# Optimization experiments

Hardware: AMD Instinct MI355X
Metric: run time of the kernel (lower is better)

## Reference

```python
import jax, jax.numpy as jnp
import numpy as np

DISC = 10  # discretizer bins
EPS = 1e-5


def _discretize(x):
    # stand-in for sklearn discretizer: uniform bins over [-3, 3] for N(0,1) data
    t = jnp.clip(jnp.floor((x + 3.0) / 6.0 * DISC), 0, DISC - 1)
    return jax.lax.stop_gradient(t).astype(jnp.int32)


def _levenshtein(tokens, features):
    # tokens: [B, L] int32, features: [Nf, F] int32 -> [B, Nf] float32
    B, L = tokens.shape
    Nf, F = features.shape
    idx = jnp.arange(L + 1, dtype=jnp.int32)
    prev0 = jnp.broadcast_to(idx, (B, Nf, L + 1)).astype(jnp.int32)

    def step(carry, fc):
        prev, j = carry  # prev: [B, Nf, L+1]
        cost = (tokens[:, None, :] != fc[None, :, None]).astype(jnp.int32)  # [B,Nf,L]
        a_rest = jnp.minimum(prev[..., 1:] + 1, prev[..., :-1] + cost)
        a0 = jnp.full((B, Nf, 1), j + 1, dtype=jnp.int32)
        a = jnp.concatenate([a0, a_rest], axis=-1)
        # cur[i] = min(a[i], cur[i-1]+1) == i + cummin(a - i)
        cur = jax.lax.cummin(a - idx, axis=2) + idx
        return (cur, j + 1), None

    (prev, _), _ = jax.lax.scan(step, (prev0, jnp.int32(0)), features.T)
    return prev[..., L].astype(jnp.float32)


def _correlations(tokens, features, L):
    # interpolate each length-F feature to length L (linear, cast to int), then pearson corr
    Nf, F = features.shape
    x_old = jnp.linspace(0.0, 1.0, F)
    x_new = jnp.linspace(0.0, 1.0, L)
    fi = jax.vmap(lambda f: jnp.interp(x_new, x_old, f.astype(jnp.float32)))(features)
    fi = fi.astype(jnp.int32).astype(jnp.float32)  # [Nf, L] (astype(int) in original)
    rf = tokens.astype(jnp.float32)  # [B, L]
    fc = fi - fi.mean(axis=-1, keepdims=True)
    rc = rf - rf.mean(axis=-1, keepdims=True)
    num = jnp.einsum('nl,bl->bn', fc, rc)
    den = jnp.linalg.norm(fc, axis=-1)[None, :] * jnp.linalg.norm(rc, axis=-1)[:, None]
    return jnp.where(den > 0, num / jnp.where(den > 0, den, 1.0), 0.0)  # [B, Nf]


def setup_inputs() -> dict:
    key = jax.random.key(0)
    k1, k2, k3 = jax.random.split(key, 3)
    B, L, Nf, F, D = 64, 512, 1024, 16, 512
    x = jax.random.normal(k1, (B, L, 1), dtype=jnp.float32)
    features = jax.random.randint(k2, (Nf, F), 0, DISC, dtype=jnp.int32)
    fan_in = 2 * 3  # in_channels * kernel
    std = np.sqrt(2.0 / (1.0 + 0.01 ** 2) / fan_in)  # kaiming, leaky_relu
    conv_w = jax.random.normal(k3, (D, 2, 3), dtype=jnp.float32) * std
    return {"x": x, "features": features, "conv_w": conv_w}


def reference(x, features, conv_w):
    B, L, _ = x.shape
    tokens = _discretize(x[..., 0])  # [B, L] int32
    dist = _levenshtein(tokens, features)  # [B, Nf]
    corr = _correlations(tokens, features, L)  # [B, Nf]
    # normalize distances over feature axis (dim=1), unbiased=False
    m = dist.mean(axis=1, keepdims=True)
    v = dist.var(axis=1, keepdims=True)
    dbg = (dist - m) / jnp.sqrt(v + EPS)
    feats2 = jnp.stack([corr, dbg], axis=1)  # [B, 2, Nf] (corr first, as torch.cat)
    # circular conv1d, kernel 3, padding 1, no bias
    inp = jnp.pad(feats2, ((0, 0), (0, 0), (1, 1)), mode='wrap')
    out = jax.lax.conv_general_dilated(inp, conv_w, (1,), 'VALID',
                                       dimension_numbers=('NCH', 'OIH', 'NCH'))  # [B, D, Nf]
    # dropout in eval mode = identity
    return jnp.transpose(out, (0, 2, 1))  # [B, Nf, D]
```

## Files before the change

kernel.cpp:

```cpp
#include <hip/hip_runtime.h>
#include <math.h>

#define NB 64
#define LL 512
#define NF 1024
#define FF 16
#define DD 512

__global__ __launch_bounds__(256) void k_prep(
    const float* __restrict__ x, const int* __restrict__ feat,
    unsigned* __restrict__ tok_pk, int* __restrict__ tsum, int* __restrict__ tsumsq,
    unsigned char* __restrict__ fiTp, int* __restrict__ fsum, int* __restrict__ fsumsq) {
  int tid = threadIdx.x;
  int blk = blockIdx.x;
  if (blk < 64) {
    int b = blk;
    __shared__ unsigned char tc[LL];
    __shared__ int redS[4], redQ[4];
    int s = 0, q = 0;
    #pragma unroll
    for (int k = 0; k < 2; ++k) {
      int l = tid + k * 256;
      float xf = x[b * LL + l];
      float c = (xf + 3.0f) / 6.0f * 10.0f;
      float tf = fminf(fmaxf(floorf(c), 0.0f), 9.0f);
      int t = (int)tf;
      tc[l] = (unsigned char)t;
      s += t; q += t * t;
    }
    #pragma unroll
    for (int o = 32; o > 0; o >>= 1) { s += __shfl_xor(s, o); q += __shfl_xor(q, o); }
    if ((tid & 63) == 0) { redS[tid >> 6] = s; redQ[tid >> 6] = q; }
    __syncthreads();
    if (tid < 128) {
      unsigned u = (unsigned)tc[tid * 4] | ((unsigned)tc[tid * 4 + 1] << 8) |
                   ((unsigned)tc[tid * 4 + 2] << 16) | ((unsigned)tc[tid * 4 + 3] << 24);
      tok_pk[b * 128 + tid] = u;
    }
    if (tid == 0) {
      tsum[b] = redS[0] + redS[1] + redS[2] + redS[3];
      tsumsq[b] = redQ[0] + redQ[1] + redQ[2] + redQ[3];
    }
  } else if (blk < 576) {
    int l = blk - 64;
    double u = (double)l * 15.0 / 511.0;
    int j = (int)u; if (j > 14) j = 14;
    double w = u - (double)j;
    size_t base = (size_t)(l >> 2) * 4096 + (size_t)(l & 3);
    #pragma unroll
    for (int k = 0; k < 4; ++k) {
      int n = tid + k * 256;
      int f0 = feat[n * FF + j], f1 = feat[n * FF + j + 1];
      int v = (int)((double)f0 + w * (double)(f1 - f0));
      fiTp[base + (size_t)n * 4] = (unsigned char)v;
    }
  } else {
    int n = blk - 576;
    __shared__ int fr[FF];
    __shared__ int rs[4], rq[4];
    if (tid < FF) fr[tid] = feat[n * FF + tid];
    __syncthreads();
    int s = 0, q = 0;
    #pragma unroll
    for (int k = 0; k < 2; ++k) {
      int l = tid + k * 256;
      double u = (double)l * 15.0 / 511.0;
      int j = (int)u; if (j > 14) j = 14;
      double w = u - (double)j;
      int f0 = fr[j], f1 = fr[j + 1];
      int v = (int)((double)f0 + w * (double)(f1 - f0));
      s += v; q += v * v;
    }
    #pragma unroll
    for (int o = 32; o > 0; o >>= 1) { s += __shfl_xor(s, o); q += __shfl_xor(q, o); }
    if ((tid & 63) == 0) { rs[tid >> 6] = s; rq[tid >> 6] = q; }
    __syncthreads();
    if (tid == 0) {
      fsum[n] = rs[0] + rs[1] + rs[2] + rs[3];
      fsumsq[n] = rq[0] + rq[1] + rq[2] + rq[3];
    }
  }
}

__global__ __launch_bounds__(256) void k_levc(
    const unsigned* __restrict__ tok_pk, const int* __restrict__ feat,
    const unsigned* __restrict__ fiTp4,
    const int* __restrict__ fsum, const int* __restrict__ fsumsq,
    const int* __restrict__ tsum, const int* __restrict__ tsumsq,
    float* __restrict__ dist, float* __restrict__ corr) {
  int tid = threadIdx.x;
  int b = blockIdx.x >> 2;
  int n = ((blockIdx.x & 3) << 8) + tid;
  __shared__ unsigned lt[128];
  __shared__ unsigned peq[10 * 256];
  if (tid < 128) lt[tid] = tok_pk[b * 128 + tid];
  int f[FF];
  const int4* f4 = reinterpret_cast<const int4*>(feat + (size_t)n * FF);
  #pragma unroll
  for (int j = 0; j < 4; ++j) {
    int4 v = f4[j];
    f[j * 4 + 0] = v.x; f[j * 4 + 1] = v.y; f[j * 4 + 2] = v.z; f[j * 4 + 3] = v.w;
  }
  #pragma unroll
  for (int c = 0; c < 10; ++c) {
    unsigned m = 0;
    #pragma unroll
    for (int j = 0; j < 16; ++j) m |= (f[j] == c) ? (1u << j) : 0u;
    peq[c * 256 + tid] = m;
  }
  __syncthreads();
  unsigned VP = 0xFFFFu, VN = 0u;
  int score = 16;
  int acc = 0;
  for (int l4 = 0; l4 < 128; ++l4) {
    unsigned u = lt[l4];
    unsigned g = fiTp4[l4 * 1024 + n];
    #pragma unroll
    for (int k = 0; k < 4; ++k) {
      unsigned t = (u >> (8 * k)) & 0xffu;
      unsigned Eq = peq[t * 256 + tid];
      unsigned D0 = (((Eq & VP) + VP) ^ VP) | Eq | VN;
      unsigned HP = VN | ~(D0 | VP);
      unsigned HN = D0 & VP;
      score += (int)((HP >> 15) & 1u);
      score -= (int)((HN >> 15) & 1u);
      unsigned X = (HP << 1) | 1u;
      VP = (HN << 1) | ~(D0 | X);
      VN = D0 & X;
      unsigned fi = (g >> (8 * k)) & 0xffu;
      acc += (int)(t * fi);
    }
  }
  dist[b * NF + n] = (float)score;
  float ts = (float)tsum[b];
  float rv = fmaxf((float)tsumsq[b] - ts * ts * (1.0f / 512.0f), 0.0f);
  float rn = sqrtf(rv);
  float fs = (float)fsum[n];
  float fv = fmaxf((float)fsumsq[n] - fs * fs * (1.0f / 512.0f), 0.0f);
  float den = sqrtf(fv) * rn;
  float num = (float)acc - fs * ts * (1.0f / 512.0f);
  corr[b * NF + n] = (den > 0.0f) ? (num / den) : 0.0f;
}

__global__ __launch_bounds__(256) void k_dstats(
    const float* __restrict__ dist, float* __restrict__ dstats) {
  int b = blockIdx.x, tid = threadIdx.x;
  double s = 0.0, q = 0.0;
  #pragma unroll
  for (int k = 0; k < 4; ++k) {
    float v = dist[b * NF + tid + k * 256];
    s += (double)v; q += (double)v * (double)v;
  }
  #pragma unroll
  for (int o = 32; o > 0; o >>= 1) { s += __shfl_xor(s, o); q += __shfl_xor(q, o); }
  __shared__ double rs[4], rq[4];
  if ((tid & 63) == 0) { rs[tid >> 6] = s; rq[tid >> 6] = q; }
  __syncthreads();
  if (tid == 0) {
    double S = rs[0] + rs[1] + rs[2] + rs[3];
    double Q = rq[0] + rq[1] + rq[2] + rq[3];
    double m = S * (1.0 / 1024.0);
    double var = Q * (1.0 / 1024.0) - m * m;
    dstats[b * 2] = (float)m;
    dstats[b * 2 + 1] = (float)(1.0 / sqrt(var + 1e-5));
  }
}

__global__ __launch_bounds__(256) void k_conv(
    const float* __restrict__ corr, const float* __restrict__ dist,
    const float* __restrict__ dstats, const float* __restrict__ w,
    float* __restrict__ out) {
  int chunk = blockIdx.x;
  int b = blockIdx.y;
  int tid = threadIdx.x;
  __shared__ float cs[66], ds_[66];
  float m = dstats[b * 2], inv = dstats[b * 2 + 1];
  if (tid < 66) {
    int ng = (chunk * 64 + tid - 1 + NF) & (NF - 1);
    cs[tid] = corr[b * NF + ng];
    ds_[tid] = (dist[b * NF + ng] - m) * inv;
  }
  __syncthreads();
  int d0 = tid * 2;
  float w0[6], w1[6];
  #pragma unroll
  for (int i = 0; i < 6; ++i) {
    w0[i] = w[d0 * 6 + i];
    w1[i] = w[(d0 + 1) * 6 + i];
  }
  const int nb = chunk * 64;
  for (int n = 0; n < 64; ++n) {
    float v0 = cs[n], v1 = cs[n + 1], v2 = cs[n + 2];
    float v3 = ds_[n], v4 = ds_[n + 1], v5 = ds_[n + 2];
    float o0 = w0[0]*v0 + w0[1]*v1 + w0[2]*v2 + w0[3]*v3 + w0[4]*v4 + w0[5]*v5;
    float o1 = w1[0]*v0 + w1[1]*v1 + w1[2]*v2 + w1[3]*v3 + w1[4]*v4 + w1[5]*v5;
    float2* op = (float2*)(out + ((size_t)(b * NF + nb + n)) * DD + d0);
    *op = make_float2(o0, o1);
  }
}

extern "C" void kernel_launch(void* const* d_in, const int* in_sizes, int n_in,
                              void* d_out, int out_size, void* d_ws, size_t ws_size,
                              hipStream_t stream) {
  const float* x = (const float*)d_in[0];
  const int* feat = (const int*)d_in[1];
  const float* w = (const float*)d_in[2];
  float* out = (float*)d_out;

  char* ws = (char*)d_ws;
  unsigned* tok_pk      = (unsigned*)(ws + 0);
  unsigned char* fiTp   = (unsigned char*)(ws + 32768);
  int* fsum             = (int*)(ws + 557056);
  int* fsumsq           = (int*)(ws + 561152);
  int* tsum             = (int*)(ws + 565248);
  int* tsumsq           = (int*)(ws + 565504);
  float* dist           = (float*)(ws + 565760);
  float* corr           = (float*)(ws + 827904);
  float* dstats         = (float*)(ws + 1090048);

  k_prep<<<1600, 256, 0, stream>>>(x, feat, tok_pk, tsum, tsumsq, fiTp, fsum, fsumsq);
  k_levc<<<256, 256, 0, stream>>>(tok_pk, feat, (const unsigned*)fiTp,
                                  fsum, fsumsq, tsum, tsumsq, dist, corr);
  k_dstats<<<NB, 256, 0, stream>>>(dist, dstats);
  k_conv<<<dim3(16, NB), 256, 0, stream>>>(corr, dist, dstats, w, out);
}
```

Measured before the change: 182.9 us.

## Transpose Myers bit-parallel Levenshtein over tokens, fuse dist stats, widen conv stores

```diff
diff --git a/kernel.cpp b/kernel.cpp
--- a/kernel.cpp
+++ b/kernel.cpp
@@ -10,7 +10,8 @@
 __global__ __launch_bounds__(256) void k_prep(
     const float* __restrict__ x, const int* __restrict__ feat,
     unsigned* __restrict__ tok_pk, int* __restrict__ tsum, int* __restrict__ tsumsq,
-    unsigned char* __restrict__ fiTp, int* __restrict__ fsum, int* __restrict__ fsumsq) {
+    unsigned char* __restrict__ fiTp, int* __restrict__ fsum, int* __restrict__ fsumsq,
+    int* __restrict__ dsum, int* __restrict__ dsumsq) {
   int tid = threadIdx.x;
   int blk = blockIdx.x;
   if (blk < 64) {
@@ -40,6 +41,7 @@
     if (tid == 0) {
       tsum[b] = redS[0] + redS[1] + redS[2] + redS[3];
       tsumsq[b] = redQ[0] + redQ[1] + redQ[2] + redQ[3];
+      dsum[b] = 0; dsumsq[b] = 0;
     }
   } else if (blk < 576) {
     int l = blk - 64;
@@ -87,12 +89,13 @@
     const unsigned* __restrict__ fiTp4,
     const int* __restrict__ fsum, const int* __restrict__ fsumsq,
     const int* __restrict__ tsum, const int* __restrict__ tsumsq,
-    float* __restrict__ dist, float* __restrict__ corr) {
+    float* __restrict__ dist, float* __restrict__ corr,
+    int* __restrict__ dsum, int* __restrict__ dsumsq) {
   int tid = threadIdx.x;
   int b = blockIdx.x >> 2;
   int n = ((blockIdx.x & 3) << 8) + tid;
   __shared__ unsigned lt[128];
-  __shared__ unsigned peq[10 * 256];
+  __shared__ unsigned peq2[16 * 16];
   if (tid < 128) lt[tid] = tok_pk[b * 128 + tid];
   int f[FF];
   const int4* f4 = reinterpret_cast<const int4*>(feat + (size_t)n * FF);
@@ -101,16 +104,19 @@
     int4 v = f4[j];
     f[j * 4 + 0] = v.x; f[j * 4 + 1] = v.y; f[j * 4 + 2] = v.z; f[j * 4 + 3] = v.w;
   }
-  #pragma unroll
-  for (int c = 0; c < 10; ++c) {
+  __syncthreads();
+  if (tid < 160) {
+    int c = tid >> 4, w = tid & 15;
     unsigned m = 0;
     #pragma unroll
-    for (int j = 0; j < 16; ++j) m |= (f[j] == c) ? (1u << j) : 0u;
-    peq[c * 256 + tid] = m;
-  }
-  __syncthreads();
-  unsigned VP = 0xFFFFu, VN = 0u;
-  int score = 16;
+    for (int jj = 0; jj < 8; ++jj) {
+      unsigned u = lt[w * 8 + jj];
+      #pragma unroll
+      for (int kk = 0; kk < 4; ++kk)
+        m |= ((int)((u >> (8 * kk)) & 0xffu) == c) ? (1u << (jj * 4 + kk)) : 0u;
+    }
+    peq2[w * 16 + c] = m;
+  }
   int acc = 0;
   for (int l4 = 0; l4 < 128; ++l4) {
     unsigned u = lt[l4];
@@ -118,20 +124,48 @@
     #pragma unroll
     for (int k = 0; k < 4; ++k) {
       unsigned t = (u >> (8 * k)) & 0xffu;
-      unsigned Eq = peq[t * 256 + tid];
-      unsigned D0 = (((Eq & VP) + VP) ^ VP) | Eq | VN;
-      unsigned HP = VN | ~(D0 | VP);
-      unsigned HN = D0 & VP;
-      score += (int)((HP >> 15) & 1u);
-      score -= (int)((HN >> 15) & 1u);
-      unsigned X = (HP << 1) | 1u;
-      VP = (HN << 1) | ~(D0 | X);
-      VN = D0 & X;
       unsigned fi = (g >> (8 * k)) & 0xffu;
       acc += (int)(t * fi);
     }
   }
+  __syncthreads();
+  unsigned VP[16], VN[16];
+  #pragma unroll
+  for (int w = 0; w < 16; ++w) { VP[w] = 0xFFFFFFFFu; VN[w] = 0u; }
+  int score = 512;
+  #pragma unroll
+  for (int j = 0; j < 16; ++j) {
+    const unsigned* pr = peq2 + f[j];
+    unsigned cadd = 0, hpin = 1, hnin = 0;
+    #pragma unroll
+    for (int w = 0; w < 16; ++w) {
+      unsigned Eq = pr[w * 16];
+      unsigned X = Eq | VN[w];
+      unsigned t = Eq & VP[w];
+      unsigned s1 = t + VP[w];
+      unsigned c1 = (s1 < t) ? 1u : 0u;
+      unsigned s = s1 + cadd;
+      unsigned c2 = (s < s1) ? 1u : 0u;
+      cadd = c1 | c2;
+      unsigned D0 = (s ^ VP[w]) | X;
+      unsigned HP = VN[w] | ~(D0 | VP[w]);
+      unsigned HN = D0 & VP[w];
+      if (w == 15) { score += (int)(HP >> 31); score -= (int)(HN >> 31); }
+      unsigned Xv = (HP << 1) | hpin;
+      hpin = HP >> 31;
+      unsigned Sn = (HN << 1) | hnin;
+      hnin = HN >> 31;
+      VP[w] = Sn | ~(D0 | Xv);
+      VN[w] = D0 & Xv;
+    }
+  }
   dist[b * NF + n] = (float)score;
+  {
+    int s = score, q = score * score;
+    #pragma unroll
+    for (int o = 32; o > 0; o >>= 1) { s += __shfl_xor(s, o); q += __shfl_xor(q, o); }
+    if ((tid & 63) == 0) { atomicAdd(&dsum[b], s); atomicAdd(&dsumsq[b], q); }
+  }
   float ts = (float)tsum[b];
   float rv = fmaxf((float)tsumsq[b] - ts * ts * (1.0f / 512.0f), 0.0f);
   float rn = sqrtf(rv);
@@ -142,60 +176,51 @@
   corr[b * NF + n] = (den > 0.0f) ? (num / den) : 0.0f;
 }
 
-__global__ __launch_bounds__(256) void k_dstats(
-    const float* __restrict__ dist, float* __restrict__ dstats) {
-  int b = blockIdx.x, tid = threadIdx.x;
-  double s = 0.0, q = 0.0;
-  #pragma unroll
-  for (int k = 0; k < 4; ++k) {
-    float v = dist[b * NF + tid + k * 256];
-    s += (double)v; q += (double)v * (double)v;
-  }
-  #pragma unroll
-  for (int o = 32; o > 0; o >>= 1) { s += __shfl_xor(s, o); q += __shfl_xor(q, o); }
-  __shared__ double rs[4], rq[4];
-  if ((tid & 63) == 0) { rs[tid >> 6] = s; rq[tid >> 6] = q; }
-  __syncthreads();
-  if (tid == 0) {
-    double S = rs[0] + rs[1] + rs[2] + rs[3];
-    double Q = rq[0] + rq[1] + rq[2] + rq[3];
-    double m = S * (1.0 / 1024.0);
-    double var = Q * (1.0 / 1024.0) - m * m;
-    dstats[b * 2] = (float)m;
-    dstats[b * 2 + 1] = (float)(1.0 / sqrt(var + 1e-5));
-  }
-}
-
 __global__ __launch_bounds__(256) void k_conv(
     const float* __restrict__ corr, const float* __restrict__ dist,
-    const float* __restrict__ dstats, const float* __restrict__ w,
-    float* __restrict__ out) {
+    const int* __restrict__ dsum, const int* __restrict__ dsumsq,
+    const float* __restrict__ w, float* __restrict__ out) {
   int chunk = blockIdx.x;
   int b = blockIdx.y;
   int tid = threadIdx.x;
-  __shared__ float cs[66], ds_[66];
-  float m = dstats[b * 2], inv = dstats[b * 2 + 1];
+  __shared__ float cs[66], dsr[66];
+  __shared__ float sm[2];
+  if (tid == 0) {
+    double S = (double)dsum[b], Q = (double)dsumsq[b];
+    double md = S * (1.0 / 1024.0);
+    double var = Q * (1.0 / 1024.0) - md * md;
+    sm[0] = (float)md;
+    sm[1] = (float)(1.0 / sqrt(var + 1e-5));
+  }
   if (tid < 66) {
     int ng = (chunk * 64 + tid - 1 + NF) & (NF - 1);
     cs[tid] = corr[b * NF + ng];
-    ds_[tid] = (dist[b * NF + ng] - m) * inv;
+    dsr[tid] = dist[b * NF + ng];
   }
   __syncthreads();
-  int d0 = tid * 2;
-  float w0[6], w1[6];
-  #pragma unroll
-  for (int i = 0; i < 6; ++i) {
-    w0[i] = w[d0 * 6 + i];
-    w1[i] = w[(d0 + 1) * 6 + i];
-  }
+  float m = sm[0], inv = sm[1];
+  int rowsel = tid >> 7;
+  int lane = tid & 127;
+  int d0 = lane * 4;
+  float wr[4][6];
+  #pragma unroll
+  for (int r = 0; r < 4; ++r)
+    #pragma unroll
+    for (int i = 0; i < 6; ++i)
+      wr[r][i] = w[(d0 + r) * 6 + i];
   const int nb = chunk * 64;
-  for (int n = 0; n < 64; ++n) {
-    float v0 = cs[n], v1 = cs[n + 1], v2 = cs[n + 2];
-    float v3 = ds_[n], v4 = ds_[n + 1], v5 = ds_[n + 2];
-    float o0 = w0[0]*v0 + w0[1]*v1 + w0[2]*v2 + w0[3]*v3 + w0[4]*v4 + w0[5]*v5;
-    float o1 = w1[0]*v0 + w1[1]*v1 + w1[2]*v2 + w1[3]*v3 + w1[4]*v4 + w1[5]*v5;
-    float2* op = (float2*)(out + ((size_t)(b * NF + nb + n)) * DD + d0);
-    *op = make_float2(o0, o1);
+  for (int n = 0; n < 64; n += 2) {
+    int nn = n + rowsel;
+    float v0 = cs[nn], v1 = cs[nn + 1], v2 = cs[nn + 2];
+    float v3 = (dsr[nn] - m) * inv;
+    float v4 = (dsr[nn + 1] - m) * inv;
+    float v5 = (dsr[nn + 2] - m) * inv;
+    float4 o;
+    o.x = wr[0][0]*v0 + wr[0][1]*v1 + wr[0][2]*v2 + wr[0][3]*v3 + wr[0][4]*v4 + wr[0][5]*v5;
+    o.y = wr[1][0]*v0 + wr[1][1]*v1 + wr[1][2]*v2 + wr[1][3]*v3 + wr[1][4]*v4 + wr[1][5]*v5;
+    o.z = wr[2][0]*v0 + wr[2][1]*v1 + wr[2][2]*v2 + wr[2][3]*v3 + wr[2][4]*v4 + wr[2][5]*v5;
+    o.w = wr[3][0]*v0 + wr[3][1]*v1 + wr[3][2]*v2 + wr[3][3]*v3 + wr[3][4]*v4 + wr[3][5]*v5;
+    *(float4*)(out + ((size_t)(b * NF + nb + nn)) * DD + d0) = o;
   }
 }
 
@@ -216,11 +241,13 @@
   int* tsumsq           = (int*)(ws + 565504);
   float* dist           = (float*)(ws + 565760);
   float* corr           = (float*)(ws + 827904);
-  float* dstats         = (float*)(ws + 1090048);
-
-  k_prep<<<1600, 256, 0, stream>>>(x, feat, tok_pk, tsum, tsumsq, fiTp, fsum, fsumsq);
+  int* dsum             = (int*)(ws + 1090048);
+  int* dsumsq           = (int*)(ws + 1090304);
+
+  k_prep<<<1600, 256, 0, stream>>>(x, feat, tok_pk, tsum, tsumsq, fiTp,
+                                   fsum, fsumsq, dsum, dsumsq);
   k_levc<<<256, 256, 0, stream>>>(tok_pk, feat, (const unsigned*)fiTp,
-                                  fsum, fsumsq, tsum, tsumsq, dist, corr);
-  k_dstats<<<NB, 256, 0, stream>>>(dist, dstats);
-  k_conv<<<dim3(16, NB), 256, 0, stream>>>(corr, dist, dstats, w, out);
-}
+                                  fsum, fsumsq, tsum, tsumsq, dist, corr,
+                                  dsum, dsumsq);
+  k_conv<<<dim3(16, NB), 256, 0, stream>>>(corr, dist, dsum, dsumsq, w, out);
+}
```

Measured after the change: 190.9 us. 1.04x slower.
